# Kernel tuning notes

Hardware: AMD Instinct MI355X
Metric: run time of the kernel (lower is better)

The kernel has to match this reference:

```python
import jax, jax.numpy as jnp
import numpy as np
from jax.scipy.special import gammaln, logsumexp

N, P, K, R = 100000, 256, 64, 16

def setup_inputs() -> dict:
    key = jax.random.key(0)
    kx, km, kp = jax.random.split(key, 3)
    X = jax.random.normal(kx, (N, P), dtype=jnp.float32)
    X = X / jnp.linalg.norm(X, axis=1, keepdims=True)  # points on the sphere S^{p-1}
    M = jax.random.normal(km, (K, P, R), dtype=jnp.float32)
    pi = jax.random.normal(kp, (K,), dtype=jnp.float32)
    return {"X": X, "M": M, "pi": pi}

def reference(X, M, pi):
    p = X.shape[1]
    r = M.shape[-1]
    half_p = 0.5 * float(p)
    # log surface area constant of the ACG normalizer
    logSA = gammaln(half_p) - jnp.log(2.0) - half_p * jnp.log(jnp.pi)
    # D = I_r + M^T M per component: [K, r, r]
    D = jnp.eye(r, dtype=M.dtype) + jnp.einsum('kpr,kps->krs', M, M)
    _, log_det_D = jnp.linalg.slogdet(D)            # [K]
    Dinv = jnp.linalg.inv(D)                        # [K, r, r]
    XM = jnp.einsum('np,kpr->knr', X, M)            # [K, N, r]
    quad = jnp.einsum('knr,krs,kns->kn', XM, Dinv, XM)  # [K, N]
    pdf = 1.0 - quad                                # Woodbury: x^T Sigma^{-1} x for unit x
    log_acg_pdf = logSA - 0.5 * log_det_D[:, None] - half_p * jnp.log(pdf)
    density = log_acg_pdf + jax.nn.log_softmax(pi)[:, None]   # [K, N]
    loglik = jnp.sum(logsumexp(density, axis=0))
    return loglik
```

## Files before the change

### kernel.cpp

```cpp
#include <hip/hip_runtime.h>
#include <hip/hip_bf16.h>
#include <math.h>

#define NPTS 100000
#define NSTRIPE 1568
#define KCOMP 64

typedef float v4f __attribute__((ext_vector_type(4)));
typedef __bf16 v8bf __attribute__((ext_vector_type(8)));
typedef __bf16 v4bf __attribute__((ext_vector_type(4)));


__global__ __launch_bounds__(256) void prep_comp(const float* __restrict__ M,
                                                 const float* __restrict__ pi,
                                                 __bf16* __restrict__ Bt,
                                                 float* __restrict__ cvec,
                                                 float logSA) {
    __shared__ float Ml[256][16];
    __shared__ float S[16][17];
    __shared__ float sh_logpi;
    const int k = blockIdx.x, t = threadIdx.x;

    const float4* src = (const float4*)(M + (size_t)k * 4096 + (size_t)t * 16);
    float4 a0 = src[0], a1 = src[1], a2 = src[2], a3 = src[3];
    ((float4*)Ml[t])[0] = a0; ((float4*)Ml[t])[1] = a1;
    ((float4*)Ml[t])[2] = a2; ((float4*)Ml[t])[3] = a3;

    if (t < 64) {
        float v = pi[t];
        float mx = v;
        for (int off = 32; off; off >>= 1) mx = fmaxf(mx, __shfl_xor(mx, off));
        float e = __expf(v - mx);
        float s = e;
        for (int off = 32; off; off >>= 1) s += __shfl_xor(s, off);
        if (t == 0) sh_logpi = pi[k] - mx - logf(s);
    }
    __syncthreads();

    {
        int r = t >> 4, c = t & 15;
        float s = (r == c) ? 1.0f : 0.0f;
        for (int p = 0; p < 256; ++p) s += Ml[p][r] * Ml[p][c];
        S[r][c] = s;
    }
    __syncthreads();

    for (int j = 0; j < 16; ++j) {
        if (t == 0) S[j][j] = sqrtf(S[j][j]);
        __syncthreads();
        if (t > j && t < 16) S[t][j] = S[t][j] / S[j][j];
        __syncthreads();
        {
            int r = t >> 4, c = t & 15;
            if (r > j && c > j && c <= r) S[r][c] -= S[r][j] * S[c][j];
        }
        __syncthreads();
    }

    if (t == 0) {
        float ldet = 0.0f;
        for (int j = 0; j < 16; ++j) ldet += logf(S[j][j]);
        cvec[k] = logSA - ldet + sh_logpi;
    }

    float m[16] = {a0.x, a0.y, a0.z, a0.w, a1.x, a1.y, a1.z, a1.w,
                   a2.x, a2.y, a2.z, a2.w, a3.x, a3.y, a3.z, a3.w};
    float y[16];
#pragma unroll
    for (int r = 0; r < 16; ++r) {
        float v = m[r];
#pragma unroll
        for (int q = 0; q < r; ++q) v -= S[r][q] * y[q];
        y[r] = v / S[r][r];
    }
    const int cw = k >> 2, n = k & 3;
    const int ks = t >> 5, e = t & 7;
    const int lbase = ((t >> 3) & 3) * 16;
#pragma unroll
    for (int r = 0; r < 16; ++r) {
        const size_t off = (size_t)cw * 16384 + (size_t)ks * 2048 + (size_t)n * 512
                         + (size_t)(lbase + r) * 8 + e;
        Bt[off] = (__bf16)y[r];
    }
}

__global__ __launch_bounds__(256) void convert_X(const float* __restrict__ X,
                                                 __bf16* __restrict__ Xb) {
    __shared__ __bf16 T[64][264];
    const int st = blockIdx.x;
    const int n0 = st * 64;
    const int t = threadIdx.x;

#pragma unroll
    for (int j = 0; j < 16; ++j) {
        const int u = j * 256 + t;
        const int r = u >> 6, c4 = u & 63;
        const int n = n0 + r;
        float4 v = make_float4(0.f, 0.f, 0.f, 0.f);
        if (n < NPTS) v = ((const float4*)X)[(size_t)n * 64 + c4];
        v4bf o = {(__bf16)v.x, (__bf16)v.y, (__bf16)v.z, (__bf16)v.w};
        *(v4bf*)&T[r][c4 * 4] = o;
    }
    __syncthreads();

#pragma unroll
    for (int ks = 0; ks < 8; ++ks) {
        const int mh = t >> 6;
        const int l = t & 63;
        const int row = mh * 16 + (l & 15);
        const int col = ks * 32 + (l >> 4) * 8;
        v8bf val = *(const v8bf*)&T[row][col];
        const size_t off = (size_t)st * 16384 + (size_t)ks * 2048
                         + (size_t)mh * 512 + (size_t)l * 8;
        *(v8bf*)(Xb + off) = val;
    }
}

__global__ __launch_bounds__(256, 2) void gemm_density(const __bf16* __restrict__ Xb,
                                                       const __bf16* __restrict__ Bt,
                                                       const float* __restrict__ cvec,
                                                       float* __restrict__ dens_t) {
    const int bid = blockIdx.x;
    const int xcd = bid & 7;
    const int w = threadIdx.x >> 6, lane = threadIdx.x & 63;
    const int widx = (bid >> 3) * 4 + w;
    if (widx >= 196) return;
    const int st = xcd * 196 + widx;
    const int laneoff = lane * 8;

    const __bf16* Ab = Xb + ((size_t)st << 14) + laneoff;
    v8bf af[8][4];
#pragma unroll
    for (int ks = 0; ks < 8; ++ks)
#pragma unroll
        for (int m = 0; m < 4; ++m)
            af[ks][m] = *(const v8bf*)(Ab + ks * 2048 + m * 512);

    const float4* cv4 = (const float4*)cvec;
    float* outbase = dens_t + ((size_t)st << 6) * 64;

#pragma unroll 1
    for (int cw = 0; cw < 16; ++cw) {
        const __bf16* Bb = Bt + ((size_t)cw << 14) + laneoff;
        v4f acc[4][4] = {};
#pragma unroll
        for (int ks = 0; ks < 8; ++ks) {
            v8bf bg[4];
#pragma unroll
            for (int n = 0; n < 4; ++n) bg[n] = *(const v8bf*)(Bb + ks * 2048 + n * 512);
#pragma unroll
            for (int m = 0; m < 4; ++m)
#pragma unroll
                for (int n = 0; n < 4; ++n)
                    acc[m][n] = __builtin_amdgcn_mfma_f32_16x16x32_bf16(bg[n], af[ks][m], acc[m][n], 0, 0, 0);
        }

        const float4 cv = cv4[cw];
#pragma unroll
        for (int m = 0; m < 4; ++m) {
            v4f dq;
#pragma unroll
            for (int n = 0; n < 4; ++n) {
                v4f qv = acc[m][n];
                float s = qv[0] * qv[0] + qv[1] * qv[1] + qv[2] * qv[2] + qv[3] * qv[3];
                s += __shfl_xor(s, 16);
                s += __shfl_xor(s, 32);
                const float c = (n == 0) ? cv.x : (n == 1) ? cv.y : (n == 2) ? cv.z : cv.w;
                dq[n] = c - 128.0f * __logf(1.0f - s);
            }
            if (lane < 16) {
                *(v4f*)(outbase + ((size_t)(m * 16 + lane) << 6) + (cw << 2)) = dq;
            }
        }
    }
}

__global__ __launch_bounds__(256) void reduce_ll(const float* __restrict__ dens_t,
                                                 float* __restrict__ out) {
    const int n = blockIdx.x * 256 + threadIdx.x;
    float local = 0.0f;
    if (n < NPTS) {
        const float4* p = (const float4*)(dens_t + ((size_t)n << 6));
        float4 d0 = p[0];
        float m = fmaxf(fmaxf(d0.x, d0.y), fmaxf(d0.z, d0.w));
        float s = __expf(d0.x - m) + __expf(d0.y - m) + __expf(d0.z - m) + __expf(d0.w - m);
#pragma unroll
        for (int j = 1; j < 16; ++j) {
            float4 d = p[j];
            float mt = fmaxf(fmaxf(d.x, d.y), fmaxf(d.z, d.w));
            float mn = fmaxf(m, mt);
            s = s * __expf(m - mn)
              + __expf(d.x - mn) + __expf(d.y - mn) + __expf(d.z - mn) + __expf(d.w - mn);
            m = mn;
        }
        local = m + __logf(s);
    }
    for (int off = 32; off; off >>= 1) local += __shfl_down(local, off);
    __shared__ float part[4];
    const int wv = threadIdx.x >> 6, lane = threadIdx.x & 63;
    if (lane == 0) part[wv] = local;
    __syncthreads();
    if (threadIdx.x == 0) atomicAdd(out, part[0] + part[1] + part[2] + part[3]);
}

extern "C" void kernel_launch(void* const* d_in, const int* in_sizes, int n_in,
                              void* d_out, int out_size, void* d_ws, size_t ws_size,
                              hipStream_t stream) {
    const float* X  = (const float*)d_in[0];
    const float* M  = (const float*)d_in[1];
    const float* pi = (const float*)d_in[2];
    float* out = (float*)d_out;

    char* ws = (char*)d_ws;
    __bf16* Xb     = (__bf16*)ws;
    __bf16* Bt     = (__bf16*)(ws + 51380224);
    float*  dens_t = (float*)(ws + 51904512);
    float*  cvec   = (float*)(ws + 77594624);

    const double half_p = 128.0;
    const float logSA = (float)(lgamma(half_p) - log(2.0) - half_p * log(M_PI));

    hipMemsetAsync(d_out, 0, sizeof(float), stream);
    prep_comp<<<64, 256, 0, stream>>>(M, pi, Bt, cvec, logSA);
    convert_X<<<1568, 256, 0, stream>>>(X, Xb);
    gemm_density<<<512, 256, 0, stream>>>(Xb, Bt, cvec, dens_t);
    reduce_ll<<<391, 256, 0, stream>>>(dens_t, out);
}
```

Before: 134.3 us.

## Fuse logsumexp reduction into GEMM kernel and double-buffer B fragment loads

The density values are no longer written to a [N,64] intermediate. The GEMM kernel now keeps an online running max and sum per point across the component chunks and atomically adds each wave's total log-likelihood, which removes the separate reduce kernel and roughly 25 MB of global writes and reads. B-fragment loads are also software-pipelined with two register buffers, prefetching the next k-step or next chunk while the MFMAs run. The first k-step uses a multiply-by-zero trick that adds a dependency so the loads are ordered, and an empty asm pins the A fragments in registers. Together these raise register pressure and could cost occupancy.

```diff
diff --git a/kernel.cpp b/kernel.cpp
--- a/kernel.cpp
+++ b/kernel.cpp
@@ -119,7 +119,7 @@
 __global__ __launch_bounds__(256, 2) void gemm_density(const __bf16* __restrict__ Xb,
                                                        const __bf16* __restrict__ Bt,
                                                        const float* __restrict__ cvec,
-                                                       float* __restrict__ dens_t) {
+                                                       float* __restrict__ out) {
     const int bid = blockIdx.x;
     const int xcd = bid & 7;
     const int w = threadIdx.x >> 6, lane = threadIdx.x & 63;
@@ -133,32 +133,59 @@
 #pragma unroll
     for (int ks = 0; ks < 8; ++ks)
 #pragma unroll
-        for (int m = 0; m < 4; ++m)
+        for (int m = 0; m < 4; ++m) {
             af[ks][m] = *(const v8bf*)(Ab + ks * 2048 + m * 512);
+            asm volatile("" : "+v"(af[ks][m]));
+        }
+
+    const __bf16* Bbase = Bt + laneoff;
+#define LOADB(dst, cw_, ks_) do {                                                \
+    const __bf16* _p = Bbase + ((size_t)(cw_) << 14) + (ks_) * 2048;             \
+    _Pragma("unroll")                                                            \
+    for (int n = 0; n < 4; ++n) dst[n] = *(const v8bf*)(_p + n * 512);           \
+} while (0)
+#define MFMA16(bg, ks) do {                                                      \
+    _Pragma("unroll")                                                            \
+    for (int m = 0; m < 4; ++m)                                                  \
+        _Pragma("unroll")                                                        \
+        for (int n = 0; n < 4; ++n)                                              \
+            acc[m][n] = __builtin_amdgcn_mfma_f32_16x16x32_bf16(bg[n], af[ks][m], acc[m][n], 0, 0, 0); \
+} while (0)
 
     const float4* cv4 = (const float4*)cvec;
-    float* outbase = dens_t + ((size_t)st << 6) * 64;
+    const v4f z4 = (v4f)(0.0f);
+
+    v8bf bgA[4], bgB[4];
+    LOADB(bgA, 0, 0);
+
+    float mrun[4] = {-INFINITY, -INFINITY, -INFINITY, -INFINITY};
+    float srun[4] = {0.f, 0.f, 0.f, 0.f};
 
 #pragma unroll 1
     for (int cw = 0; cw < 16; ++cw) {
-        const __bf16* Bb = Bt + ((size_t)cw << 14) + laneoff;
-        v4f acc[4][4] = {};
-#pragma unroll
-        for (int ks = 0; ks < 8; ++ks) {
-            v8bf bg[4];
-#pragma unroll
-            for (int n = 0; n < 4; ++n) bg[n] = *(const v8bf*)(Bb + ks * 2048 + n * 512);
-#pragma unroll
-            for (int m = 0; m < 4; ++m)
-#pragma unroll
-                for (int n = 0; n < 4; ++n)
-                    acc[m][n] = __builtin_amdgcn_mfma_f32_16x16x32_bf16(bg[n], af[ks][m], acc[m][n], 0, 0, 0);
+        v4f acc[4][4];
+        LOADB(bgB, cw, 1);
+#pragma unroll
+        for (int m = 0; m < 4; ++m)
+#pragma unroll
+            for (int n = 0; n < 4; ++n)
+                acc[m][n] = __builtin_amdgcn_mfma_f32_16x16x32_bf16(bgB[n] * (__bf16)0.f + bgA[n], af[0][m], z4, 0, 0, 0);
+        LOADB(bgA, cw, 2);
+        MFMA16(bgB, 1);
+#pragma unroll
+        for (int kp = 1; kp < 4; ++kp) {
+            const int k0 = kp * 2, k1 = kp * 2 + 1;
+            LOADB(bgB, cw, k1);
+            MFMA16(bgA, k0);
+            if (k1 < 7) { LOADB(bgA, cw, k1 + 1); }
+            else if (cw < 15) { LOADB(bgA, cw + 1, 0); }
+            MFMA16(bgB, k1);
         }
 
         const float4 cv = cv4[cw];
 #pragma unroll
         for (int m = 0; m < 4; ++m) {
-            v4f dq;
+            float d[4];
 #pragma unroll
             for (int n = 0; n < 4; ++n) {
                 v4f qv = acc[m][n];
@@ -166,41 +193,31 @@
                 s += __shfl_xor(s, 16);
                 s += __shfl_xor(s, 32);
                 const float c = (n == 0) ? cv.x : (n == 1) ? cv.y : (n == 2) ? cv.z : cv.w;
-                dq[n] = c - 128.0f * __logf(1.0f - s);
+                d[n] = c - 128.0f * __logf(1.0f - s);
             }
-            if (lane < 16) {
-                *(v4f*)(outbase + ((size_t)(m * 16 + lane) << 6) + (cw << 2)) = dq;
-            }
-        }
-    }
-}
-
-__global__ __launch_bounds__(256) void reduce_ll(const float* __restrict__ dens_t,
-                                                 float* __restrict__ out) {
-    const int n = blockIdx.x * 256 + threadIdx.x;
-    float local = 0.0f;
-    if (n < NPTS) {
-        const float4* p = (const float4*)(dens_t + ((size_t)n << 6));
-        float4 d0 = p[0];
-        float m = fmaxf(fmaxf(d0.x, d0.y), fmaxf(d0.z, d0.w));
-        float s = __expf(d0.x - m) + __expf(d0.y - m) + __expf(d0.z - m) + __expf(d0.w - m);
-#pragma unroll
-        for (int j = 1; j < 16; ++j) {
-            float4 d = p[j];
-            float mt = fmaxf(fmaxf(d.x, d.y), fmaxf(d.z, d.w));
-            float mn = fmaxf(m, mt);
-            s = s * __expf(m - mn)
-              + __expf(d.x - mn) + __expf(d.y - mn) + __expf(d.z - mn) + __expf(d.w - mn);
-            m = mn;
-        }
-        local = m + __logf(s);
-    }
-    for (int off = 32; off; off >>= 1) local += __shfl_down(local, off);
-    __shared__ float part[4];
-    const int wv = threadIdx.x >> 6, lane = threadIdx.x & 63;
-    if (lane == 0) part[wv] = local;
-    __syncthreads();
-    if (threadIdx.x == 0) atomicAdd(out, part[0] + part[1] + part[2] + part[3]);
+            const float mt = fmaxf(fmaxf(d[0], d[1]), fmaxf(d[2], d[3]));
+            const float mn = fmaxf(mrun[m], mt);
+            srun[m] = srun[m] * __expf(mrun[m] - mn)
+                    + __expf(d[0] - mn) + __expf(d[1] - mn)
+                    + __expf(d[2] - mn) + __expf(d[3] - mn);
+            mrun[m] = mn;
+        }
+    }
+#undef LOADB
+#undef MFMA16
+
+    float tot = 0.f;
+#pragma unroll
+    for (int m = 0; m < 4; ++m) {
+        const int pt = st * 64 + m * 16 + (lane & 15);
+        const float lse = mrun[m] + __logf(srun[m]);
+        tot += (pt < NPTS) ? lse : 0.f;
+    }
+    tot += __shfl_xor(tot, 1);
+    tot += __shfl_xor(tot, 2);
+    tot += __shfl_xor(tot, 4);
+    tot += __shfl_xor(tot, 8);
+    if (lane == 0) atomicAdd(out, tot);
 }
 
 extern "C" void kernel_launch(void* const* d_in, const int* in_sizes, int n_in,
@@ -212,10 +229,9 @@
     float* out = (float*)d_out;
 
     char* ws = (char*)d_ws;
-    __bf16* Xb     = (__bf16*)ws;
-    __bf16* Bt     = (__bf16*)(ws + 51380224);
-    float*  dens_t = (float*)(ws + 51904512);
-    float*  cvec   = (float*)(ws + 77594624);
+    __bf16* Xb   = (__bf16*)ws;
+    __bf16* Bt   = (__bf16*)(ws + 51380224);
+    float*  cvec = (float*)(ws + 51904512);
 
     const double half_p = 128.0;
     const float logSA = (float)(lgamma(half_p) - log(2.0) - half_p * log(M_PI));
@@ -223,6 +239,5 @@
     hipMemsetAsync(d_out, 0, sizeof(float), stream);
     prep_comp<<<64, 256, 0, stream>>>(M, pi, Bt, cvec, logSA);
     convert_X<<<1568, 256, 0, stream>>>(X, Xb);
-    gemm_density<<<512, 256, 0, stream>>>(Xb, Bt, cvec, dens_t);
-    reduce_ll<<<391, 256, 0, stream>>>(dens_t, out);
-}
+    gemm_density<<<512, 256, 0, stream>>>(Xb, Bt, cvec, out);
+}
```

New measurement: 148.1 us. 1.1x slower.

## Fuse logsumexp into GEMM epilogue and split components across waves

Applied to the files above, without the earlier changes.

Each GEMM wave now keeps an online running max and sum over its components instead of writing the full K=64 density matrix, and the final reduce only merges two (max, sum) pairs per point. Components are split into two halves across paired waves, which doubles the waves per stripe. The A fragments are now loaded per k-step rather than held in registers, and B loads are software-prefetched two k-steps ahead. This removes the roughly 25MB density write and re-read and raises occupancy (launch bounds 4). The cost is that the X stripe is read twice, once per half, and the loop now issues more global loads.

```diff
diff --git a/kernel.cpp b/kernel.cpp
--- a/kernel.cpp
+++ b/kernel.cpp
@@ -7,6 +7,7 @@
 #define KCOMP 64
 
 typedef float v4f __attribute__((ext_vector_type(4)));
+typedef float v2f __attribute__((ext_vector_type(2)));
 typedef __bf16 v8bf __attribute__((ext_vector_type(8)));
 typedef __bf16 v4bf __attribute__((ext_vector_type(4)));
 
@@ -116,84 +117,100 @@
     }
 }
 
-__global__ __launch_bounds__(256, 2) void gemm_density(const __bf16* __restrict__ Xb,
+__global__ __launch_bounds__(256, 4) void gemm_density(const __bf16* __restrict__ Xb,
                                                        const __bf16* __restrict__ Bt,
                                                        const float* __restrict__ cvec,
-                                                       float* __restrict__ dens_t) {
+                                                       float* __restrict__ pairs) {
     const int bid = blockIdx.x;
-    const int xcd = bid & 7;
+    const int xcd = bid & 7, i = bid >> 3;
     const int w = threadIdx.x >> 6, lane = threadIdx.x & 63;
-    const int widx = (bid >> 3) * 4 + w;
-    if (widx >= 196) return;
-    const int st = xcd * 196 + widx;
-    const int laneoff = lane * 8;
-
-    const __bf16* Ab = Xb + ((size_t)st << 14) + laneoff;
-    v8bf af[8][4];
-#pragma unroll
-    for (int ks = 0; ks < 8; ++ks)
-#pragma unroll
-        for (int m = 0; m < 4; ++m)
-            af[ks][m] = *(const v8bf*)(Ab + ks * 2048 + m * 512);
-
+    const int st = xcd * 196 + i * 2 + (w >> 1);
+    const int h = w & 1;
+    const int cw0 = h * 8;
+    const int lo = lane & 15;
+    const int n0 = st * 64;
+
+    const __bf16* Ab = Xb + ((size_t)st << 14) + lane * 8;
+    const __bf16* Bb = Bt + lane * 8;
+
+#define LOADB(dst, cw_, ks_) do {                                          \
+    const __bf16* _p = Bb + ((size_t)(cw_) << 14) + ((size_t)(ks_) << 11); \
+    dst[0] = *(const v8bf*)(_p);                                           \
+    dst[1] = *(const v8bf*)(_p + 512);                                     \
+    dst[2] = *(const v8bf*)(_p + 1024);                                    \
+    dst[3] = *(const v8bf*)(_p + 1536);                                    \
+} while (0)
+
+    v8bf bg[4][4];
+    LOADB(bg[0], cw0, 0);
+    LOADB(bg[1], cw0, 1);
+
+    float mrun[4] = {-INFINITY, -INFINITY, -INFINITY, -INFINITY};
+    float srun[4] = {0.f, 0.f, 0.f, 0.f};
     const float4* cv4 = (const float4*)cvec;
-    float* outbase = dens_t + ((size_t)st << 6) * 64;
 
 #pragma unroll 1
-    for (int cw = 0; cw < 16; ++cw) {
-        const __bf16* Bb = Bt + ((size_t)cw << 14) + laneoff;
+    for (int c = 0; c < 8; ++c) {
+        const int cw = cw0 + c;
         v4f acc[4][4] = {};
 #pragma unroll
         for (int ks = 0; ks < 8; ++ks) {
-            v8bf bg[4];
-#pragma unroll
-            for (int n = 0; n < 4; ++n) bg[n] = *(const v8bf*)(Bb + ks * 2048 + n * 512);
+            const int pk = ks + 2;
+            const int pcw = (pk < 8) ? cw : (cw0 + ((c + 1) & 7));
+            LOADB(bg[pk & 3], pcw, pk & 7);
+            v8bf af[4];
 #pragma unroll
             for (int m = 0; m < 4; ++m)
+                af[m] = *(const v8bf*)(Ab + ks * 2048 + m * 512);
+#pragma unroll
+            for (int m = 0; m < 4; ++m)
 #pragma unroll
                 for (int n = 0; n < 4; ++n)
-                    acc[m][n] = __builtin_amdgcn_mfma_f32_16x16x32_bf16(bg[n], af[ks][m], acc[m][n], 0, 0, 0);
+                    acc[m][n] = __builtin_amdgcn_mfma_f32_16x16x32_bf16(
+                        bg[ks & 3][n], af[m], acc[m][n], 0, 0, 0);
         }
 
         const float4 cv = cv4[cw];
 #pragma unroll
         for (int m = 0; m < 4; ++m) {
-            v4f dq;
+            float d[4];
 #pragma unroll
             for (int n = 0; n < 4; ++n) {
                 v4f qv = acc[m][n];
                 float s = qv[0] * qv[0] + qv[1] * qv[1] + qv[2] * qv[2] + qv[3] * qv[3];
                 s += __shfl_xor(s, 16);
                 s += __shfl_xor(s, 32);
-                const float c = (n == 0) ? cv.x : (n == 1) ? cv.y : (n == 2) ? cv.z : cv.w;
-                dq[n] = c - 128.0f * __logf(1.0f - s);
+                const float cc = (n == 0) ? cv.x : (n == 1) ? cv.y : (n == 2) ? cv.z : cv.w;
+                d[n] = cc - 128.0f * __logf(1.0f - s);
             }
-            if (lane < 16) {
-                *(v4f*)(outbase + ((size_t)(m * 16 + lane) << 6) + (cw << 2)) = dq;
-            }
-        }
-    }
-}
-
-__global__ __launch_bounds__(256) void reduce_ll(const float* __restrict__ dens_t,
-                                                 float* __restrict__ out) {
+            const float mt = fmaxf(fmaxf(d[0], d[1]), fmaxf(d[2], d[3]));
+            const float mn = fmaxf(mrun[m], mt);
+            srun[m] = srun[m] * __expf(mrun[m] - mn)
+                    + __expf(d[0] - mn) + __expf(d[1] - mn)
+                    + __expf(d[2] - mn) + __expf(d[3] - mn);
+            mrun[m] = mn;
+        }
+    }
+#undef LOADB
+
+    if (lane < 16) {
+#pragma unroll
+        for (int m = 0; m < 4; ++m) {
+            const int pt = n0 + m * 16 + lo;
+            v2f p; p[0] = mrun[m]; p[1] = srun[m];
+            *(v2f*)(pairs + (size_t)pt * 4 + h * 2) = p;
+        }
+    }
+}
+
+__global__ __launch_bounds__(256) void merge_ll(const float* __restrict__ pairs,
+                                                float* __restrict__ out) {
     const int n = blockIdx.x * 256 + threadIdx.x;
     float local = 0.0f;
     if (n < NPTS) {
-        const float4* p = (const float4*)(dens_t + ((size_t)n << 6));
-        float4 d0 = p[0];
-        float m = fmaxf(fmaxf(d0.x, d0.y), fmaxf(d0.z, d0.w));
-        float s = __expf(d0.x - m) + __expf(d0.y - m) + __expf(d0.z - m) + __expf(d0.w - m);
-#pragma unroll
-        for (int j = 1; j < 16; ++j) {
-            float4 d = p[j];
-            float mt = fmaxf(fmaxf(d.x, d.y), fmaxf(d.z, d.w));
-            float mn = fmaxf(m, mt);
-            s = s * __expf(m - mn)
-              + __expf(d.x - mn) + __expf(d.y - mn) + __expf(d.z - mn) + __expf(d.w - mn);
-            m = mn;
-        }
-        local = m + __logf(s);
+        const float4 p = *(const float4*)(pairs + (size_t)n * 4);
+        const float M = fmaxf(p.x, p.z);
+        local = M + __logf(p.y * __expf(p.x - M) + p.w * __expf(p.z - M));
     }
     for (int off = 32; off; off >>= 1) local += __shfl_down(local, off);
     __shared__ float part[4];
@@ -212,10 +229,10 @@
     float* out = (float*)d_out;
 
     char* ws = (char*)d_ws;
-    __bf16* Xb     = (__bf16*)ws;
-    __bf16* Bt     = (__bf16*)(ws + 51380224);
-    float*  dens_t = (float*)(ws + 51904512);
-    float*  cvec   = (float*)(ws + 77594624);
+    __bf16* Xb    = (__bf16*)ws;
+    __bf16* Bt    = (__bf16*)(ws + 51380224);
+    float*  cvec  = (float*)(ws + 51904512);
+    float*  pairs = (float*)(ws + 51905024);
 
     const double half_p = 128.0;
     const float logSA = (float)(lgamma(half_p) - log(2.0) - half_p * log(M_PI));
@@ -223,6 +240,6 @@
     hipMemsetAsync(d_out, 0, sizeof(float), stream);
     prep_comp<<<64, 256, 0, stream>>>(M, pi, Bt, cvec, logSA);
     convert_X<<<1568, 256, 0, stream>>>(X, Xb);
-    gemm_density<<<512, 256, 0, stream>>>(Xb, Bt, cvec, dens_t);
-    reduce_ll<<<391, 256, 0, stream>>>(dens_t, out);
-}
+    gemm_density<<<784, 256, 0, stream>>>(Xb, Bt, cvec, pairs);
+    merge_ll<<<392, 256, 0, stream>>>(pairs, out);
+}
```

Measured after the change: 252.8 us. +88.3%, slower.
